# Performance work log

Measured on AMD Instinct MI355X. Metric: run time of the kernel, lower is better.

The kernel has to match this reference:

```python
import jax, jax.numpy as jnp
import numpy as np

FACTOR = 2
FIR = (1.0, 3.0, 3.0, 1.0)  # resample_kernel from fir_kernel=(1,3,3,1)


def _fir_kernel_2d(dtype):
    # StyleGAN2 _setup_kernel: outer product, normalize, then * gain * factor^2
    k = np.asarray(FIR, dtype=np.float64)
    k = np.outer(k, k)
    k /= k.sum()
    k *= FACTOR ** 2
    return jnp.asarray(k, dtype)


def setup_inputs() -> dict:
    key = jax.random.key(0)
    kx, kw, kb = jax.random.split(key, 3)
    B, H, W, C, O = 16, 64, 64, 128, 128
    x = jax.random.normal(kx, (B, H, W, C), jnp.float32)
    fan_avg = (3 * 3 * C + 3 * 3 * O) / 2.0  # default_init ~ variance_scaling fan_avg
    w = jax.random.normal(kw, (3, 3, C, O), jnp.float32) * np.float32(np.sqrt(1.0 / fan_avg))
    b = jax.random.normal(kb, (O,), jnp.float32) * 0.1
    return {"x": x, "w": w, "b": b}


def reference(x, w, b):
    B, H, W, C = x.shape
    kh = w.shape[0]  # 3
    # Step 1: stride-2 transposed conv, VALID. tf.nn.conv2d_transpose with the
    # double-flipped/transposed weights reduces exactly to plain correlation of
    # the zero-dilated input with w (HWIO).  -> (B, 2H+1, 2W+1, O)
    y = jax.lax.conv_general_dilated(
        x, w,
        window_strides=(1, 1),
        padding=((kh - 1, kh - 1), (kh - 1, kh - 1)),
        lhs_dilation=(FACTOR, FACTOR),
        dimension_numbers=('NHWC', 'HWIO', 'NHWC'))
    # Step 2: depthwise FIR filtering (upfirdn2d with up=down=1 and the fused pads)
    k2d = _fir_kernel_2d(x.dtype)
    kwid = k2d.shape[0]  # 4
    p = (kwid - FACTOR) - (kh - 1)          # = 0
    pad0 = (p + 1) // 2 + FACTOR - 1        # = 1
    pad1 = p // 2 + 1                       # = 1
    O = y.shape[-1]
    # upfirdn uses true convolution -> flip kernel (symmetric here, but faithful)
    fir = jnp.tile(k2d[::-1, ::-1][:, :, None, None], (1, 1, 1, O))
    y = jax.lax.conv_general_dilated(
        y, fir,
        window_strides=(1, 1),
        padding=((pad0, pad1), (pad0, pad1)),
        dimension_numbers=('NHWC', 'HWIO', 'NHWC'),
        feature_group_count=O)              # (B, 2H, 2W, O)
    return y + b.reshape(1, 1, 1, -1)
```

## Files before the change

kernel.cpp:

```cpp
#include <hip/hip_runtime.h>
#include <hip/hip_bf16.h>

#define BB 16
#define HH 64
#define WW 64
#define CC 128
#define OO 128

typedef __attribute__((ext_vector_type(8))) short bf16x8;
typedef __attribute__((ext_vector_type(4))) float f32x4;

__constant__ float Kc[2][3][3] = {
    {{0.75f, 0.25f, 0.00f}, {0.25f, 0.75f, 0.75f}, {0.00f, 0.00f, 0.25f}},
    {{0.25f, 0.00f, 0.00f}, {0.75f, 0.75f, 0.25f}, {0.00f, 0.25f, 0.75f}},
};

__device__ __forceinline__ unsigned short f2bf(float f) {
    union { float f; unsigned u; } a; a.f = f;
    unsigned r = a.u + 0x7fffu + ((a.u >> 16) & 1u);
    return (unsigned short)(r >> 16);
}

__global__ void pack_b_kernel(const float* __restrict__ w, unsigned short* __restrict__ bp) {
    int l  = threadIdx.x;
    int nf = blockIdx.x;
    int ks = blockIdx.y;
    int ph = blockIdx.z;
    int ps = ph >> 1, pt = ph & 1;
    int didj = ks >> 2;
    int di = didj / 3, dj = didj % 3;
    float kk[3][3];
    #pragma unroll
    for (int a = 0; a < 3; ++a)
        #pragma unroll
        for (int bq = 0; bq < 3; ++bq)
            kk[a][bq] = Kc[ps][di][a] * Kc[pt][dj][bq];

    int o = nf * 16 + (l & 15);
    int chunk = l >> 4;
    int cbase = (ks & 3) * 32 + chunk * 8;
    size_t off = ((((size_t)ph * 36 + ks) * 8 + nf) * 64 + l) * 8;
    #pragma unroll
    for (int j = 0; j < 8; ++j) {
        int c = cbase + j;
        float acc = 0.f;
        #pragma unroll
        for (int a = 0; a < 3; ++a)
            #pragma unroll
            for (int bq = 0; bq < 3; ++bq)
                acc += kk[a][bq] * w[((a * 3 + bq) * CC + c) * OO + o];
        bp[off + j] = f2bf(acc);
    }
}

__launch_bounds__(256, 2)
__global__ void upconv_kernel(const float* __restrict__ x,
                              const unsigned short* __restrict__ bp,
                              const float* __restrict__ bias,
                              float* __restrict__ out) {
    __shared__ unsigned short xs[6 * 18 * 128];

    const int tid = threadIdx.x;
    const int gT0 = blockIdx.x * 16;
    const int gS0 = blockIdx.y * 4;
    const int b   = blockIdx.z;

    for (int i = tid; i < 6 * 18 * 16; i += 256) {
        int c8  = i & 15;
        int rc  = i >> 4;
        int col = rc % 18;
        int r   = rc / 18;
        int gr = gS0 - 1 + r;
        int gc = gT0 - 1 + col;
        float4 v0 = make_float4(0.f, 0.f, 0.f, 0.f);
        float4 v1 = v0;
        if ((unsigned)gr < HH && (unsigned)gc < WW) {
            const float* p = x + (((size_t)b * HH + gr) * WW + gc) * CC + c8 * 8;
            v0 = *(const float4*)p;
            v1 = *(const float4*)(p + 4);
        }
        unsigned short tmp[8];
        tmp[0] = f2bf(v0.x); tmp[1] = f2bf(v0.y); tmp[2] = f2bf(v0.z); tmp[3] = f2bf(v0.w);
        tmp[4] = f2bf(v1.x); tmp[5] = f2bf(v1.y); tmp[6] = f2bf(v1.z); tmp[7] = f2bf(v1.w);
        int byte = (((r * 18 + col) * 128 + c8 * 8) * 2) ^ ((col & 7) << 4);
        *(bf16x8*)((char*)xs + byte) = *(const bf16x8*)tmp;
    }
    __syncthreads();

    const int wid    = tid >> 6;
    const int l      = tid & 63;
    const int lane15 = l & 15;
    const int chunk  = l >> 4;
    const int ps = wid >> 1, pt = wid & 1;

    f32x4 acc[4][8];
    #pragma unroll
    for (int mi = 0; mi < 4; ++mi)
        #pragma unroll
        for (int ni = 0; ni < 8; ++ni)
            acc[mi][ni] = (f32x4){0.f, 0.f, 0.f, 0.f};

    const bf16x8* bpv = (const bf16x8*)bp + (size_t)wid * 36 * 8 * 64;

    bf16x8 b0[4];
    {
        const bf16x8* bk = bpv + l;
        #pragma unroll
        for (int ni = 0; ni < 4; ++ni) b0[ni] = bk[ni * 64];
    }

    #pragma unroll 4
    for (int ks = 0; ks < 36; ++ks) {
        const bf16x8* bk = bpv + (size_t)ks * 512 + l;
        bf16x8 b1[4];
        #pragma unroll
        for (int ni = 0; ni < 4; ++ni) b1[ni] = bk[(ni + 4) * 64];

        int didj = ks >> 2;
        int di = didj / 3, dj = didj % 3;
        int c0 = (ks & 3) * 32 + chunk * 8;
        bf16x8 af[4];
        #pragma unroll
        for (int mi = 0; mi < 4; ++mi) {
            int r   = mi + di;
            int col = lane15 + dj;
            int byte = (((r * 18 + col) * 128 + c0) * 2) ^ ((col & 7) << 4);
            af[mi] = *(const bf16x8*)((const char*)xs + byte);
        }

        #pragma unroll
        for (int ni = 0; ni < 4; ++ni)
            #pragma unroll
            for (int mi = 0; mi < 4; ++mi)
                acc[mi][ni] = __builtin_amdgcn_mfma_f32_16x16x32_bf16(af[mi], b0[ni], acc[mi][ni], 0, 0, 0);

        bf16x8 bn[4];
        if (ks + 1 < 36) {
            const bf16x8* bk2 = bpv + (size_t)(ks + 1) * 512 + l;
            #pragma unroll
            for (int ni = 0; ni < 4; ++ni) bn[ni] = bk2[ni * 64];
        }

        #pragma unroll
        for (int ni = 0; ni < 4; ++ni)
            #pragma unroll
            for (int mi = 0; mi < 4; ++mi)
                acc[mi][ni + 4] = __builtin_amdgcn_mfma_f32_16x16x32_bf16(af[mi], b1[ni], acc[mi][ni + 4], 0, 0, 0);

        #pragma unroll
        for (int ni = 0; ni < 4; ++ni) b0[ni] = bn[ni];
    }

    #pragma unroll
    for (int ni = 0; ni < 8; ++ni) {
        int o = ni * 16 + lane15;
        float bv = bias[o];
        #pragma unroll
        for (int mi = 0; mi < 4; ++mi) {
            int s = 2 * (gS0 + mi) + ps;
            #pragma unroll
            for (int rg = 0; rg < 4; ++rg) {
                int t = 2 * (gT0 + chunk * 4 + rg) + pt;
                __builtin_nontemporal_store(acc[mi][ni][rg] + bv,
                    &out[(((size_t)b * 128 + s) * 128 + t) * 128 + o]);
            }
        }
    }
}

extern "C" void kernel_launch(void* const* d_in, const int* in_sizes, int n_in,
                              void* d_out, int out_size, void* d_ws, size_t ws_size,
                              hipStream_t stream) {
    const float* x    = (const float*)d_in[0];
    const float* w    = (const float*)d_in[1];
    const float* bias = (const float*)d_in[2];
    float* out        = (float*)d_out;
    unsigned short* bp = (unsigned short*)d_ws;

    dim3 gp(8, 36, 4);
    pack_b_kernel<<<gp, 64, 0, stream>>>(w, bp);

    dim3 gm(4, 16, 16);
    upconv_kernel<<<gm, 256, 0, stream>>>(x, bp, bias, out);
}
```

Baseline: 237.7 us.

## Split output phases across blocks and stage shared B tiles in LDS

Each block now handles a single output phase and an 8-row input tile, with the 4 waves splitting rows instead of phases. The per-phase B weights are staged through a double-buffered LDS tile shared by all waves, replacing per-wave global loads. This is meant to cut redundant global B traffic and halve accumulator registers, possibly allowing more occupancy. In exchange, each x tile is now converted and loaded by 4 blocks (one per phase), and a __syncthreads runs every k-step.

```diff
diff --git a/kernel.cpp b/kernel.cpp
--- a/kernel.cpp
+++ b/kernel.cpp
@@ -58,14 +58,23 @@
                               const unsigned short* __restrict__ bp,
                               const float* __restrict__ bias,
                               float* __restrict__ out) {
-    __shared__ unsigned short xs[6 * 18 * 128];
+    __shared__ unsigned short xs[10 * 18 * 128];
+    __shared__ unsigned short bs[2][4096];
 
     const int tid = threadIdx.x;
     const int gT0 = blockIdx.x * 16;
-    const int gS0 = blockIdx.y * 4;
-    const int b   = blockIdx.z;
+    const int gS0 = blockIdx.y * 8;
+    const int bz  = blockIdx.z;
+    const int b   = bz >> 2;
+    const int ph  = bz & 3;
+    const int ps  = ph >> 1, pt = ph & 1;
 
-    for (int i = tid; i < 6 * 18 * 16; i += 256) {
+    const bf16x8* bsrc = (const bf16x8*)bp + (size_t)ph * 36 * 512;
+
+    bf16x8 st0 = bsrc[tid];
+    bf16x8 st1 = bsrc[tid + 256];
+
+    for (int i = tid; i < 10 * 18 * 16; i += 256) {
         int c8  = i & 15;
         int rc  = i >> 4;
         int col = rc % 18;
@@ -85,70 +94,64 @@
         int byte = (((r * 18 + col) * 128 + c8 * 8) * 2) ^ ((col & 7) << 4);
         *(bf16x8*)((char*)xs + byte) = *(const bf16x8*)tmp;
     }
+
+    {
+        bf16x8* bw = (bf16x8*)bs[0];
+        bw[tid] = st0;
+        bw[tid + 256] = st1;
+    }
     __syncthreads();
 
     const int wid    = tid >> 6;
     const int l      = tid & 63;
     const int lane15 = l & 15;
     const int chunk  = l >> 4;
-    const int ps = wid >> 1, pt = wid & 1;
 
-    f32x4 acc[4][8];
+    f32x4 acc[2][8];
     #pragma unroll
-    for (int mi = 0; mi < 4; ++mi)
+    for (int mi = 0; mi < 2; ++mi)
         #pragma unroll
         for (int ni = 0; ni < 8; ++ni)
             acc[mi][ni] = (f32x4){0.f, 0.f, 0.f, 0.f};
 
-    const bf16x8* bpv = (const bf16x8*)bp + (size_t)wid * 36 * 8 * 64;
-
-    bf16x8 b0[4];
-    {
-        const bf16x8* bk = bpv + l;
-        #pragma unroll
-        for (int ni = 0; ni < 4; ++ni) b0[ni] = bk[ni * 64];
-    }
-
     #pragma unroll 4
     for (int ks = 0; ks < 36; ++ks) {
-        const bf16x8* bk = bpv + (size_t)ks * 512 + l;
-        bf16x8 b1[4];
-        #pragma unroll
-        for (int ni = 0; ni < 4; ++ni) b1[ni] = bk[(ni + 4) * 64];
+        const int cur = ks & 1;
+
+        bf16x8 n0, n1;
+        if (ks + 1 < 36) {
+            n0 = bsrc[(size_t)(ks + 1) * 512 + tid];
+            n1 = bsrc[(size_t)(ks + 1) * 512 + tid + 256];
+        }
 
         int didj = ks >> 2;
         int di = didj / 3, dj = didj % 3;
         int c0 = (ks & 3) * 32 + chunk * 8;
-        bf16x8 af[4];
+
+        bf16x8 af[2];
         #pragma unroll
-        for (int mi = 0; mi < 4; ++mi) {
-            int r   = mi + di;
+        for (int mi = 0; mi < 2; ++mi) {
+            int r   = 2 * wid + mi + di;
             int col = lane15 + dj;
             int byte = (((r * 18 + col) * 128 + c0) * 2) ^ ((col & 7) << 4);
             af[mi] = *(const bf16x8*)((const char*)xs + byte);
         }
 
+        const bf16x8* bl = (const bf16x8*)bs[cur];
         #pragma unroll
-        for (int ni = 0; ni < 4; ++ni)
+        for (int ni = 0; ni < 8; ++ni) {
+            bf16x8 bfv = bl[ni * 64 + l];
             #pragma unroll
-            for (int mi = 0; mi < 4; ++mi)
-                acc[mi][ni] = __builtin_amdgcn_mfma_f32_16x16x32_bf16(af[mi], b0[ni], acc[mi][ni], 0, 0, 0);
-
-        bf16x8 bn[4];
-        if (ks + 1 < 36) {
-            const bf16x8* bk2 = bpv + (size_t)(ks + 1) * 512 + l;
-            #pragma unroll
-            for (int ni = 0; ni < 4; ++ni) bn[ni] = bk2[ni * 64];
+            for (int mi = 0; mi < 2; ++mi)
+                acc[mi][ni] = __builtin_amdgcn_mfma_f32_16x16x32_bf16(af[mi], bfv, acc[mi][ni], 0, 0, 0);
         }
 
-        #pragma unroll
-        for (int ni = 0; ni < 4; ++ni)
-            #pragma unroll
-            for (int mi = 0; mi < 4; ++mi)
-                acc[mi][ni + 4] = __builtin_amdgcn_mfma_f32_16x16x32_bf16(af[mi], b1[ni], acc[mi][ni + 4], 0, 0, 0);
-
-        #pragma unroll
-        for (int ni = 0; ni < 4; ++ni) b0[ni] = bn[ni];
+        if (ks + 1 < 36) {
+            bf16x8* bw = (bf16x8*)bs[cur ^ 1];
+            bw[tid] = n0;
+            bw[tid + 256] = n1;
+        }
+        __syncthreads();
     }
 
     #pragma unroll
@@ -156,8 +159,8 @@
         int o = ni * 16 + lane15;
         float bv = bias[o];
         #pragma unroll
-        for (int mi = 0; mi < 4; ++mi) {
-            int s = 2 * (gS0 + mi) + ps;
+        for (int mi = 0; mi < 2; ++mi) {
+            int s = 2 * (gS0 + 2 * wid + mi) + ps;
             #pragma unroll
             for (int rg = 0; rg < 4; ++rg) {
                 int t = 2 * (gT0 + chunk * 4 + rg) + pt;
@@ -180,6 +183,6 @@
     dim3 gp(8, 36, 4);
     pack_b_kernel<<<gp, 64, 0, stream>>>(w, bp);
 
-    dim3 gm(4, 16, 16);
+    dim3 gm(4, 8, 64);
     upconv_kernel<<<gm, 256, 0, stream>>>(x, bp, bias, out);
 }
```

Result: slower. 256.5 us (+7.9%).
